# Kernel optimization log

Measured on AMD Instinct MI355X. Metric: run time of the kernel, lower is better.

Reference implementation:

```python
import jax, jax.numpy as jnp
import numpy as np

SCALE = 256 ** -0.5  # d_proj ** -0.5

def setup_inputs() -> dict:
    key = jax.random.key(0)
    k1, k2, k3, k4 = jax.random.split(key, 4)
    B, L, T = 8, 2048, 512
    Dh, Dg, Dp = 1024, 768, 256
    H = jax.random.normal(k1, (B, L, Dh), dtype=jnp.float32)
    G = jax.random.normal(k2, (B, T, Dg), dtype=jnp.float32)
    mask = jnp.zeros((B, L), dtype=jnp.int32)  # True/nonzero = masked OUT
    Wk = jax.random.normal(k3, (Dh, Dp), dtype=jnp.float32) * (Dh ** -0.5)
    Wq = jax.random.normal(k4, (Dg, Dp), dtype=jnp.float32) * (Dg ** -0.5)
    return {"H": H, "G": G, "mask": mask, "Wk": Wk, "Wq": Wq}

def reference(H, G, mask, Wk, Wq):
    # K: [B,L,Dp], Q: [B,T,Dp]
    K = jnp.einsum('bld,dp->blp', H, Wk)
    Q = jnp.einsum('btd,dp->btp', G, Wq)
    # logits over keys L: [B,T,L]
    logits = jnp.einsum('btp,blp->btl', Q, K) * SCALE
    logits = jnp.where(mask[:, None, :] != 0, -jnp.inf, logits)
    alpha = jax.nn.softmax(logits, axis=-1)  # online-softmax in torch == exact softmax
    Z = jnp.einsum('btl,bld->btd', alpha, H)  # [B,T,Dh]
    return Z
```

## Files before the change

kernel.cpp:

```cpp
#include <hip/hip_runtime.h>
#include <math.h>

#define BATCH 8
#define LKEYS 2048
#define TQ    512
#define DH    1024
#define DG    768
#define DP    256
#define SCALE 0.0625f

typedef short  short8  __attribute__((ext_vector_type(8)));
typedef float  floatx4 __attribute__((ext_vector_type(4)));
typedef unsigned short u16x4 __attribute__((ext_vector_type(4)));
typedef unsigned short u16x8 __attribute__((ext_vector_type(8)));

typedef unsigned int __attribute__((address_space(1))) as1_uint;
typedef unsigned int __attribute__((address_space(3))) as3_uint;

__device__ __forceinline__ unsigned short f2b(float f) {
    union { float f; unsigned int u; } v; v.f = f;
    unsigned int u = v.u;
    unsigned int r = u + 0x7fffu + ((u >> 16) & 1u);
    if ((u & 0x7f800000u) == 0x7f800000u) r = u;
    return (unsigned short)(r >> 16);
}
__device__ __forceinline__ float b2f(unsigned short b) {
    union { unsigned int u; float f; } v; v.u = ((unsigned int)b) << 16;
    return v.f;
}

__device__ __forceinline__ void gload_lds16(const void* g, void* l) {
    __builtin_amdgcn_global_load_lds((const as1_uint*)g, (as3_uint*)l, 16, 0, 0);
}

__host__ __device__ constexpr int wcnt_vm(int vm) {
    return (vm & 15) | (7 << 4) | (15 << 8);
}

template<int BM, int BN, int OMODE, int SWZ, int KS>
__global__ __launch_bounds__(256) void gemm_bf16_p(
    const unsigned short* __restrict__ Ap, const unsigned short* __restrict__ Bp,
    const int* __restrict__ maskp, void* __restrict__ Cp,
    int K, int lda, int ldb, int ldc,
    long sA, long sB, long sC, long sM, long sP, float scale)
{
    constexpr int FM = BM / 32, FN = BN / 32;
    constexpr int AI = BM / 64, BI = BN / 64;
    constexpr int NL = AI + BI;

    __shared__ unsigned short As[4][BM * 32];
    __shared__ unsigned short Bs[4][BN * 32];

    int bx = blockIdx.x, by = blockIdx.y, zz = blockIdx.z;
    if (SWZ == 1) {
        const int gx = gridDim.x;
        const int nwg = gx * gridDim.y;
        const int f = by * gx + bx;
        const int nper = nwg >> 3;
        const int fl = (f & 7) * nper + (f >> 3);
        bx = fl % gx; by = fl / gx;
    } else if (SWZ == 2) {
        const int gx = gridDim.x, nxy = gridDim.x * gridDim.y;
        const long l = blockIdx.x + (long)gx * (blockIdx.y + (long)gridDim.y * blockIdx.z);
        const int xcd  = (int)(l & 7);
        const int slot = (int)(l >> 3);
        zz = xcd + 8 * (slot / nxy);
        const int rem = slot % nxy;
        bx = rem % gx; by = rem / gx;
    }
    const int z    = (KS > 1) ? (zz & 7) : zz;
    const int part = (KS > 1) ? (zz >> 3) : 0;
    const int koff = part * K;

    const int tid  = threadIdx.x;
    const int lane = tid & 63;
    const int wid  = tid >> 6;
    const int wr   = wid >> 1, wc = wid & 1;
    const int lrow = lane & 15;
    const int g    = lane >> 4;

    const unsigned short* A = Ap + (long)z * sA + (long)(by * BM) * lda + koff;
    const unsigned short* B = Bp + (long)z * sB + (long)(bx * BN) * ldb + koff;
    const int srow = tid >> 2, sslot = tid & 3;

    const int nt = K / 32;
    floatx4 acc[FM][FN] = {};

    auto stage = [&](int t, int b) {
        const int k0 = t * 32;
        #pragma unroll
        for (int i = 0; i < AI; ++i)
            gload_lds16(A + (long)(srow + i * 64) * lda + k0 + sslot * 8,
                        (void*)&As[b][(i * 256 + tid) * 8]);
        #pragma unroll
        for (int i = 0; i < BI; ++i)
            gload_lds16(B + (long)(srow + i * 64) * ldb + k0 + sslot * 8,
                        (void*)&Bs[b][(i * 256 + tid) * 8]);
    };

    stage(0, 0);
    stage(1, 1);
    for (int t = 0; t < nt; ++t) {
        if (t + 2 < nt) {
            stage(t + 2, (t + 2) & 3);
            __builtin_amdgcn_s_waitcnt(wcnt_vm(2 * NL));
        } else if (t + 1 < nt) {
            __builtin_amdgcn_s_waitcnt(wcnt_vm(NL));
        } else {
            __builtin_amdgcn_s_waitcnt(wcnt_vm(0));
        }
        __builtin_amdgcn_s_barrier();
        __builtin_amdgcn_sched_barrier(0);

        const int b = t & 3;
        short8 a[FM], bf[FN];
        #pragma unroll
        for (int m = 0; m < FM; ++m)
            a[m] = *(const short8*)&As[b][(wr * (BM / 2) + m * 16 + lrow) * 32 + g * 8];
        #pragma unroll
        for (int n = 0; n < FN; ++n)
            bf[n] = *(const short8*)&Bs[b][(wc * (BN / 2) + n * 16 + lrow) * 32 + g * 8];
        __builtin_amdgcn_s_setprio(1);
        #pragma unroll
        for (int m = 0; m < FM; ++m)
            #pragma unroll
            for (int n = 0; n < FN; ++n)
                acc[m][n] = __builtin_amdgcn_mfma_f32_16x16x32_bf16(
                    a[m], bf[n], acc[m][n], 0, 0, 0);
        __builtin_amdgcn_s_setprio(0);
        __builtin_amdgcn_sched_barrier(0);
    }

    const int orow = by * BM + wr * (BM / 2);
    const int ocol = bx * BN + wc * (BN / 2);
    if (OMODE == 0) {
        float* C = (float*)Cp + (long)z * sC + (long)part * sP;
        #pragma unroll
        for (int m = 0; m < FM; ++m)
            #pragma unroll
            for (int n = 0; n < FN; ++n)
                #pragma unroll
                for (int r = 0; r < 4; ++r)
                    C[(long)(orow + m * 16 + 4 * g + r) * ldc + ocol + n * 16 + lrow]
                        = acc[m][n][r];
    } else if (OMODE == 1) {
        unsigned short* C = (unsigned short*)Cp + (long)z * sC + (long)part * sP;
        #pragma unroll
        for (int m = 0; m < FM; ++m)
            #pragma unroll
            for (int n = 0; n < FN; ++n)
                #pragma unroll
                for (int r = 0; r < 4; ++r)
                    C[(long)(orow + m * 16 + 4 * g + r) * ldc + ocol + n * 16 + lrow]
                        = f2b(acc[m][n][r]);
    } else if (OMODE == 2) {
        const int* mask = maskp + (long)z * sM;
        float* C = (float*)Cp + (long)z * sC;
        #pragma unroll
        for (int n = 0; n < FN; ++n) {
            int c = ocol + n * 16 + lrow;
            bool masked = (mask[c] != 0);
            #pragma unroll
            for (int m = 0; m < FM; ++m)
                #pragma unroll
                for (int r = 0; r < 4; ++r)
                    C[(long)(orow + m * 16 + 4 * g + r) * ldc + c]
                        = masked ? -INFINITY : acc[m][n][r] * scale;
        }
    } else {
        const int* mask = maskp + (long)z * sM;
        unsigned short* C = (unsigned short*)Cp + (long)z * sC;
        #pragma unroll
        for (int n = 0; n < FN; ++n) {
            int c = ocol + n * 16 + lrow;
            bool masked = (mask[c] != 0);
            #pragma unroll
            for (int m = 0; m < FM; ++m)
                #pragma unroll
                for (int r = 0; r < 4; ++r)
                    C[(long)(orow + m * 16 + 4 * g + r) * ldc + c]
                        = masked ? (unsigned short)0xFF80u
                                 : f2b(acc[m][n][r] * scale);
        }
    }
}

__global__ __launch_bounds__(256) void proj_kq(
    const unsigned short* __restrict__ Hb, const unsigned short* __restrict__ WkT,
    unsigned short* __restrict__ Kb,
    const unsigned short* __restrict__ Gb, const unsigned short* __restrict__ WqT,
    unsigned short* __restrict__ Qb)
{
    constexpr int BM = 128, BN = 64, FM = 4, FN = 2, AI = 2, BI = 1, NL = 3;
    __shared__ unsigned short As[4][BM * 32];
    __shared__ unsigned short Bs[4][BN * 32];

    const int f  = blockIdx.y * 4 + blockIdx.x;
    const int fl = (f & 7) * 80 + (f >> 3);
    const int bx = fl & 3, by = fl >> 2;

    const unsigned short *A, *B;
    unsigned short* C;
    int K, ld;
    if (by < 128) { A = Hb + (long)by * 128 * DH;          B = WkT; C = Kb; K = DH; ld = DH; }
    else          { A = Gb + (long)(by - 128) * 128 * DG;  B = WqT; C = Qb; K = DG; ld = DG; }
    B += (long)bx * BN * ld;
    const int orow0 = (by < 128) ? by * 128 : (by - 128) * 128;

    const int tid  = threadIdx.x;
    const int lane = tid & 63;
    const int wid  = tid >> 6;
    const int wr   = wid >> 1, wc = wid & 1;
    const int lrow = lane & 15;
    const int g    = lane >> 4;
    const int srow = tid >> 2, sslot = tid & 3;

    const int nt = K / 32;
    floatx4 acc[FM][FN] = {};

    auto stage = [&](int t, int b) {
        const int k0 = t * 32;
        #pragma unroll
        for (int i = 0; i < AI; ++i)
            gload_lds16(A + (long)(srow + i * 64) * ld + k0 + sslot * 8,
                        (void*)&As[b][(i * 256 + tid) * 8]);
        gload_lds16(B + (long)srow * ld + k0 + sslot * 8,
                    (void*)&Bs[b][tid * 8]);
    };

    stage(0, 0);
    stage(1, 1);
    for (int t = 0; t < nt; ++t) {
        if (t + 2 < nt) {
            stage(t + 2, (t + 2) & 3);
            __builtin_amdgcn_s_waitcnt(wcnt_vm(2 * NL));
        } else if (t + 1 < nt) {
            __builtin_amdgcn_s_waitcnt(wcnt_vm(NL));
        } else {
            __builtin_amdgcn_s_waitcnt(wcnt_vm(0));
        }
        __builtin_amdgcn_s_barrier();
        __builtin_amdgcn_sched_barrier(0);

        const int b = t & 3;
        short8 a[FM], bf[FN];
        #pragma unroll
        for (int m = 0; m < FM; ++m)
            a[m] = *(const short8*)&As[b][(wr * 64 + m * 16 + lrow) * 32 + g * 8];
        #pragma unroll
        for (int n = 0; n < FN; ++n)
            bf[n] = *(const short8*)&Bs[b][(wc * 32 + n * 16 + lrow) * 32 + g * 8];
        __builtin_amdgcn_s_setprio(1);
        #pragma unroll
        for (int m = 0; m < FM; ++m)
            #pragma unroll
            for (int n = 0; n < FN; ++n)
                acc[m][n] = __builtin_amdgcn_mfma_f32_16x16x32_bf16(
                    a[m], bf[n], acc[m][n], 0, 0, 0);
        __builtin_amdgcn_s_setprio(0);
        __builtin_amdgcn_sched_barrier(0);
    }

    const int orow = orow0 + wr * 64;
    const int ocol = bx * BN + wc * 32;
    #pragma unroll
    for (int m = 0; m < FM; ++m)
        #pragma unroll
        for (int n = 0; n < FN; ++n)
            #pragma unroll
            for (int r = 0; r < 4; ++r)
                C[(long)(orow + m * 16 + 4 * g + r) * DP + ocol + n * 16 + lrow]
                    = f2b(acc[m][n][r]);
}

#define NH_BLK  16384
#define NG_BLK  1536
#define NWK_BLK 256
#define NWQ_BLK 192

__global__ __launch_bounds__(256) void prep_all(
    const float* __restrict__ H, const float* __restrict__ G,
    const float* __restrict__ Wk, const float* __restrict__ Wq,
    unsigned short* __restrict__ Hb, unsigned short* __restrict__ HbT,
    unsigned short* __restrict__ Gb,
    unsigned short* __restrict__ WkT, unsigned short* __restrict__ WqT)
{
    __shared__ float tf[32][33];
    const int id = blockIdx.x;

    if (id < NH_BLK) {
        const int z  = id >> 11;
        const int r_ = id & 2047;
        const int d0 = (r_ >> 6) << 5;
        const int l0 = (r_ & 63) << 5;
        const float* Hz = H + (long)z * LKEYS * DH;
        unsigned short* Hbz = Hb + (long)z * LKEYS * DH;
        unsigned short* Tz  = HbT + (long)z * DH * LKEYS;
        const int r = threadIdx.x >> 3, c = threadIdx.x & 7;
        float4 v = *(const float4*)&Hz[(long)(l0 + r) * DH + d0 + 4 * c];
        u16x4 w;
        w[0] = f2b(v.x); w[1] = f2b(v.y); w[2] = f2b(v.z); w[3] = f2b(v.w);
        *(u16x4*)&Hbz[(long)(l0 + r) * DH + d0 + 4 * c] = w;
        tf[r][4 * c + 0] = v.x; tf[r][4 * c + 1] = v.y;
        tf[r][4 * c + 2] = v.z; tf[r][4 * c + 3] = v.w;
        __syncthreads();
        u16x4 o;
        o[0] = f2b(tf[4 * c + 0][r]); o[1] = f2b(tf[4 * c + 1][r]);
        o[2] = f2b(tf[4 * c + 2][r]); o[3] = f2b(tf[4 * c + 3][r]);
        *(u16x4*)&Tz[(long)(d0 + r) * LKEYS + l0 + 4 * c] = o;
    } else if (id < NH_BLK + NG_BLK) {
        const int bid = id - NH_BLK;
        long i = ((long)bid * 256 + threadIdx.x) * 8;
        float4 a = *(const float4*)&G[i];
        float4 b = *(const float4*)&G[i + 4];
        u16x8 w;
        w[0] = f2b(a.x); w[1] = f2b(a.y); w[2] = f2b(a.z); w[3] = f2b(a.w);
        w[4] = f2b(b.x); w[5] = f2b(b.y); w[6] = f2b(b.z); w[7] = f2b(b.w);
        *(u16x8*)&Gb[i] = w;
    } else {
        const float* W; unsigned short* WT; int D, d0, p0;
        if (id < NH_BLK + NG_BLK + NWK_BLK) {
            const int bid = id - NH_BLK - NG_BLK;
            W = Wk; WT = WkT; D = DH;
            d0 = (bid & 31) * 32; p0 = (bid >> 5) * 32;
        } else {
            const int bid = id - NH_BLK - NG_BLK - NWK_BLK;
            W = Wq; WT = WqT; D = DG;
            d0 = (bid % 24) * 32; p0 = (bid / 24) * 32;
        }
        const int tx = threadIdx.x & 31, ty = threadIdx.x >> 5;
        #pragma unroll
        for (int j = 0; j < 4; ++j)
            tf[ty + 8 * j][tx] = W[(long)(d0 + ty + 8 * j) * DP + p0 + tx];
        __syncthreads();
        #pragma unroll
        for (int j = 0; j < 4; ++j)
            WT[(long)(p0 + ty + 8 * j) * D + d0 + tx] = f2b(tf[tx][ty + 8 * j]);
    }
}

__global__ __launch_bounds__(256) void reduce_add2(
    const unsigned short* __restrict__ P, long sP, float* __restrict__ Zo)
{
    long i = ((long)blockIdx.x * 256 + threadIdx.x) * 8;
    u16x8 a = *(const u16x8*)&P[i];
    u16x8 b = *(const u16x8*)&P[i + sP];
    float4 o0, o1;
    o0.x = b2f(a[0]) + b2f(b[0]);
    o0.y = b2f(a[1]) + b2f(b[1]);
    o0.z = b2f(a[2]) + b2f(b[2]);
    o0.w = b2f(a[3]) + b2f(b[3]);
    o1.x = b2f(a[4]) + b2f(b[4]);
    o1.y = b2f(a[5]) + b2f(b[5]);
    o1.z = b2f(a[6]) + b2f(b[6]);
    o1.w = b2f(a[7]) + b2f(b[7]);
    *(float4*)&Zo[i] = o0;
    *(float4*)&Zo[i + 4] = o1;
}

__global__ __launch_bounds__(256) void softmax_kernel(
    const unsigned short* __restrict__ S, unsigned short* __restrict__ Ab)
{
    const u16x8* row8 = (const u16x8*)(S + (long)blockIdx.x * LKEYS);
    u16x8* out8 = (u16x8*)(Ab + (long)blockIdx.x * LKEYS);
    const int tid = threadIdx.x;
    __shared__ float red[4];

    u16x8 v = row8[tid];
    float x[8];
    #pragma unroll
    for (int j = 0; j < 8; ++j) x[j] = b2f(v[j]);

    float m = fmaxf(fmaxf(fmaxf(x[0], x[1]), fmaxf(x[2], x[3])),
                    fmaxf(fmaxf(x[4], x[5]), fmaxf(x[6], x[7])));
    #pragma unroll
    for (int off = 32; off > 0; off >>= 1) m = fmaxf(m, __shfl_xor(m, off));
    if ((tid & 63) == 0) red[tid >> 6] = m;
    __syncthreads();
    m = fmaxf(fmaxf(red[0], red[1]), fmaxf(red[2], red[3]));

    float e[8], s = 0.f;
    #pragma unroll
    for (int j = 0; j < 8; ++j) { e[j] = __expf(x[j] - m); s += e[j]; }
    #pragma unroll
    for (int off = 32; off > 0; off >>= 1) s += __shfl_xor(s, off);
    __syncthreads();
    if ((tid & 63) == 0) red[tid >> 6] = s;
    __syncthreads();
    s = red[0] + red[1] + red[2] + red[3];

    float inv = 1.0f / s;
    u16x8 o;
    #pragma unroll
    for (int j = 0; j < 8; ++j) o[j] = f2b(e[j] * inv);
    out8[tid] = o;
}

extern "C" void kernel_launch(void* const* d_in, const int* in_sizes, int n_in,
                              void* d_out, int out_size, void* d_ws, size_t ws_size,
                              hipStream_t stream)
{
    const float* H    = (const float*)d_in[0];
    const float* G    = (const float*)d_in[1];
    const int*   mask = (const int*)  d_in[2];
    const float* Wk   = (const float*)d_in[3];
    const float* Wq   = (const float*)d_in[4];
    float*       Z    = (float*)d_out;

    unsigned short* WkT = (unsigned short*)d_ws;
    unsigned short* WqT = WkT + 262144;
    unsigned short* Ab  = WqT + 196608;
    unsigned short* Kb  = Ab  + 8388608;
    unsigned short* Qb  = Kb  + 4194304;
    unsigned short* Gb  = Qb  + 1048576;
    unsigned short* HbT = Gb  + 3145728;
    unsigned short* Hb  = HbT + 16777216;
    unsigned short* S   = Hb;
    unsigned short* Zp  = Hb;
    const long sZp = (long)BATCH * TQ * DH;
    const long sZb = (long)TQ * DH;

    prep_all<<<NH_BLK + NG_BLK + NWK_BLK + NWQ_BLK, 256, 0, stream>>>(
        H, G, Wk, Wq, Hb, HbT, Gb, WkT, WqT);

    proj_kq<<<dim3(4, 160, 1), 256, 0, stream>>>(Hb, WkT, Kb, Gb, WqT, Qb);

    gemm_bf16_p<128, 128, 3, 2, 1><<<dim3(16, 4, BATCH), 256, 0, stream>>>(
        Qb, Kb, mask, S, DP, DP, DP, LKEYS,
        (long)TQ * DP, (long)LKEYS * DP, (long)TQ * LKEYS, (long)LKEYS, 0, SCALE);

    softmax_kernel<<<BATCH * TQ, 256, 0, stream>>>(S, Ab);

    gemm_bf16_p<128, 128, 1, 2, 2><<<dim3(8, 4, 2 * BATCH), 256, 0, stream>>>(
        Ab, HbT, nullptr, Zp, LKEYS / 2, LKEYS, LKEYS, DH,
        (long)TQ * LKEYS, (long)DH * LKEYS, sZb, 0, sZp, 1.f);

    reduce_add2<<<(int)(sZp / 8 / 256), 256, 0, stream>>>(Zp, sZp, Z);
}
```

Before: 109.5 us.

## Move H transpose from prep kernel into projection kernel as extra blocks

The H bf16 transpose (HbT) is removed from prep_all, which now does a plain vectorized fp32->bf16 conversion of H and G. The transpose is instead computed from the bf16 Hb in 64x64 LDS tiles by extra blocks appended to the K/Q projection launch, so it runs alongside the GEMM blocks. The prep pass becomes a simpler streaming conversion, and the transpose reads half-width bf16 data rather than fp32. In exchange, Hb is read once more, and the transpose blocks compete with the projection GEMM for compute units and bandwidth. The wait-count helper also gains encoding for the upper vmcnt bits.

New measurement: 101.6 us (median of 2 runs). -7.2%, faster.

```diff
diff --git a/kernel.cpp b/kernel.cpp
--- a/kernel.cpp
+++ b/kernel.cpp
@@ -34,7 +34,7 @@
 }
 
 __host__ __device__ constexpr int wcnt_vm(int vm) {
-    return (vm & 15) | (7 << 4) | (15 << 8);
+    return (vm & 15) | ((vm >> 4) << 14) | (7 << 4) | (15 << 8);
 }
 
 template<int BM, int BN, int OMODE, int SWZ, int KS>
@@ -185,17 +185,49 @@
     }
 }
 
-__global__ __launch_bounds__(256) void proj_kq(
+#define NPROJ 640
+
+__global__ __launch_bounds__(256) void proj_kq_ht(
     const unsigned short* __restrict__ Hb, const unsigned short* __restrict__ WkT,
     unsigned short* __restrict__ Kb,
     const unsigned short* __restrict__ Gb, const unsigned short* __restrict__ WqT,
-    unsigned short* __restrict__ Qb)
-{
-    constexpr int BM = 128, BN = 64, FM = 4, FN = 2, AI = 2, BI = 1, NL = 3;
-    __shared__ unsigned short As[4][BM * 32];
-    __shared__ unsigned short Bs[4][BN * 32];
-
-    const int f  = blockIdx.y * 4 + blockIdx.x;
+    unsigned short* __restrict__ Qb,
+    unsigned short* __restrict__ HbT)
+{
+    __shared__ unsigned short smem[4 * 128 * 32 + 4 * 64 * 32];
+    const int tid = threadIdx.x;
+
+    if (blockIdx.x >= NPROJ) {
+        auto ts = (unsigned short(*)[68])smem;
+        const int b  = blockIdx.x - NPROJ;
+        const int z  = b >> 9;
+        const int r_ = b & 511;
+        const int l0 = (r_ >> 4) << 6;
+        const int d0 = (r_ & 15) << 6;
+        const unsigned short* Hz = Hb + (long)z * LKEYS * DH;
+        unsigned short* Tz = HbT + (long)z * DH * LKEYS;
+        #pragma unroll
+        for (int j = 0; j < 4; ++j) {
+            int idx = tid + j * 256, r = idx >> 4, c4 = idx & 15;
+            *(u16x4*)&ts[r][4 * c4] = *(const u16x4*)&Hz[(long)(l0 + r) * DH + d0 + 4 * c4];
+        }
+        __syncthreads();
+        #pragma unroll
+        for (int j = 0; j < 4; ++j) {
+            int idx = tid + j * 256, r = idx >> 4, c4 = idx & 15;
+            u16x4 o;
+            o[0] = ts[4 * c4 + 0][r]; o[1] = ts[4 * c4 + 1][r];
+            o[2] = ts[4 * c4 + 2][r]; o[3] = ts[4 * c4 + 3][r];
+            *(u16x4*)&Tz[(long)(d0 + r) * LKEYS + l0 + 4 * c4] = o;
+        }
+        return;
+    }
+
+    constexpr int FM = 4, FN = 2, AI = 2, NL = 3;
+    auto As = (unsigned short(*)[128 * 32])smem;
+    auto Bs = (unsigned short(*)[64 * 32])(smem + 4 * 128 * 32);
+
+    const int f  = blockIdx.x;
     const int fl = (f & 7) * 80 + (f >> 3);
     const int bx = fl & 3, by = fl >> 2;
 
@@ -204,10 +236,9 @@
     int K, ld;
     if (by < 128) { A = Hb + (long)by * 128 * DH;          B = WkT; C = Kb; K = DH; ld = DH; }
     else          { A = Gb + (long)(by - 128) * 128 * DG;  B = WqT; C = Qb; K = DG; ld = DG; }
-    B += (long)bx * BN * ld;
+    B += (long)bx * 64 * ld;
     const int orow0 = (by < 128) ? by * 128 : (by - 128) * 128;
 
-    const int tid  = threadIdx.x;
     const int lane = tid & 63;
     const int wid  = tid >> 6;
     const int wr   = wid >> 1, wc = wid & 1;
@@ -262,7 +293,7 @@
     }
 
     const int orow = orow0 + wr * 64;
-    const int ocol = bx * BN + wc * 32;
+    const int ocol = bx * 64 + wc * 32;
     #pragma unroll
     for (int m = 0; m < FM; ++m)
         #pragma unroll
@@ -273,7 +304,7 @@
                     = f2b(acc[m][n][r]);
 }
 
-#define NH_BLK  16384
+#define NHS_BLK 8192
 #define NG_BLK  1536
 #define NWK_BLK 256
 #define NWQ_BLK 192
@@ -281,50 +312,31 @@
 __global__ __launch_bounds__(256) void prep_all(
     const float* __restrict__ H, const float* __restrict__ G,
     const float* __restrict__ Wk, const float* __restrict__ Wq,
-    unsigned short* __restrict__ Hb, unsigned short* __restrict__ HbT,
-    unsigned short* __restrict__ Gb,
+    unsigned short* __restrict__ Hb, unsigned short* __restrict__ Gb,
     unsigned short* __restrict__ WkT, unsigned short* __restrict__ WqT)
 {
     __shared__ float tf[32][33];
     const int id = blockIdx.x;
 
-    if (id < NH_BLK) {
-        const int z  = id >> 11;
-        const int r_ = id & 2047;
-        const int d0 = (r_ >> 6) << 5;
-        const int l0 = (r_ & 63) << 5;
-        const float* Hz = H + (long)z * LKEYS * DH;
-        unsigned short* Hbz = Hb + (long)z * LKEYS * DH;
-        unsigned short* Tz  = HbT + (long)z * DH * LKEYS;
-        const int r = threadIdx.x >> 3, c = threadIdx.x & 7;
-        float4 v = *(const float4*)&Hz[(long)(l0 + r) * DH + d0 + 4 * c];
-        u16x4 w;
-        w[0] = f2b(v.x); w[1] = f2b(v.y); w[2] = f2b(v.z); w[3] = f2b(v.w);
-        *(u16x4*)&Hbz[(long)(l0 + r) * DH + d0 + 4 * c] = w;
-        tf[r][4 * c + 0] = v.x; tf[r][4 * c + 1] = v.y;
-        tf[r][4 * c + 2] = v.z; tf[r][4 * c + 3] = v.w;
-        __syncthreads();
-        u16x4 o;
-        o[0] = f2b(tf[4 * c + 0][r]); o[1] = f2b(tf[4 * c + 1][r]);
-        o[2] = f2b(tf[4 * c + 2][r]); o[3] = f2b(tf[4 * c + 3][r]);
-        *(u16x4*)&Tz[(long)(d0 + r) * LKEYS + l0 + 4 * c] = o;
-    } else if (id < NH_BLK + NG_BLK) {
-        const int bid = id - NH_BLK;
-        long i = ((long)bid * 256 + threadIdx.x) * 8;
-        float4 a = *(const float4*)&G[i];
-        float4 b = *(const float4*)&G[i + 4];
+    if (id < NHS_BLK + NG_BLK) {
+        const float* src; unsigned short* dst; long base;
+        if (id < NHS_BLK) { src = H; dst = Hb; base = (long)id * 2048; }
+        else              { src = G; dst = Gb; base = (long)(id - NHS_BLK) * 2048; }
+        long i = base + (long)threadIdx.x * 8;
+        float4 a = *(const float4*)&src[i];
+        float4 b = *(const float4*)&src[i + 4];
         u16x8 w;
         w[0] = f2b(a.x); w[1] = f2b(a.y); w[2] = f2b(a.z); w[3] = f2b(a.w);
         w[4] = f2b(b.x); w[5] = f2b(b.y); w[6] = f2b(b.z); w[7] = f2b(b.w);
-        *(u16x8*)&Gb[i] = w;
+        *(u16x8*)&dst[i] = w;
     } else {
         const float* W; unsigned short* WT; int D, d0, p0;
-        if (id < NH_BLK + NG_BLK + NWK_BLK) {
-            const int bid = id - NH_BLK - NG_BLK;
+        if (id < NHS_BLK + NG_BLK + NWK_BLK) {
+            const int bid = id - NHS_BLK - NG_BLK;
             W = Wk; WT = WkT; D = DH;
             d0 = (bid & 31) * 32; p0 = (bid >> 5) * 32;
         } else {
-            const int bid = id - NH_BLK - NG_BLK - NWK_BLK;
+            const int bid = id - NHS_BLK - NG_BLK - NWK_BLK;
             W = Wq; WT = WqT; D = DG;
             d0 = (bid % 24) * 32; p0 = (bid / 24) * 32;
         }
@@ -420,10 +432,10 @@
     const long sZp = (long)BATCH * TQ * DH;
     const long sZb = (long)TQ * DH;
 
-    prep_all<<<NH_BLK + NG_BLK + NWK_BLK + NWQ_BLK, 256, 0, stream>>>(
-        H, G, Wk, Wq, Hb, HbT, Gb, WkT, WqT);
-
-    proj_kq<<<dim3(4, 160, 1), 256, 0, stream>>>(Hb, WkT, Kb, Gb, WqT, Qb);
+    prep_all<<<NHS_BLK + NG_BLK + NWK_BLK + NWQ_BLK, 256, 0, stream>>>(
+        H, G, Wk, Wq, Hb, Gb, WkT, WqT);
+
+    proj_kq_ht<<<NPROJ + 4096, 256, 0, stream>>>(Hb, WkT, Kb, Gb, WqT, Qb, HbT);
 
     gemm_bf16_p<128, 128, 3, 2, 1><<<dim3(16, 4, BATCH), 256, 0, stream>>>(
         Qb, Kb, mask, S, DP, DP, DP, LKEYS,
```
